# Kernel optimization log

Hardware: AMD Instinct MI355X
Metric: run time of the kernel (lower is better)

Reference implementation:

```python
import jax, jax.numpy as jnp
import numpy as np

B, T, IO = 64, 1024, 1
H = 512
DELAY = 1


def _lstm_cell(x_t, h, c, Wih, Whh, bih, bhh):
    # PyTorch LSTMCell: gates = x@Wih.T + bih + h@Whh.T + bhh, gate order i,f,g,o
    gates = x_t @ Wih.T + bih + h @ Whh.T + bhh  # [B, 4H]
    i, f, g, o = jnp.split(gates, 4, axis=-1)
    i = jax.nn.sigmoid(i)
    f = jax.nn.sigmoid(f)
    g = jnp.tanh(g)
    o = jax.nn.sigmoid(o)
    c_new = f * c + i * g
    h_new = o * jnp.tanh(c_new)
    return h_new, c_new


def setup_inputs() -> dict:
    key = jax.random.key(0)
    ks = jax.random.split(key, 14)
    s = 0.02
    inp = {
        "x": jax.random.normal(ks[0], (B, T, IO), dtype=jnp.float32),
        # layer 0: input IO -> H
        "Wih0": jax.random.normal(ks[1], (4 * H, IO), dtype=jnp.float32) * s,
        "Whh0": jax.random.normal(ks[2], (4 * H, H), dtype=jnp.float32) * s,
        "bih0": jax.random.normal(ks[3], (4 * H,), dtype=jnp.float32) * s,
        "bhh0": jax.random.normal(ks[4], (4 * H,), dtype=jnp.float32) * s,
        # layer 1: H -> H
        "Wih1": jax.random.normal(ks[5], (4 * H, H), dtype=jnp.float32) * s,
        "Whh1": jax.random.normal(ks[6], (4 * H, H), dtype=jnp.float32) * s,
        "bih1": jax.random.normal(ks[7], (4 * H,), dtype=jnp.float32) * s,
        "bhh1": jax.random.normal(ks[8], (4 * H,), dtype=jnp.float32) * s,
        # layer 2: H -> H
        "Wih2": jax.random.normal(ks[9], (4 * H, H), dtype=jnp.float32) * s,
        "Whh2": jax.random.normal(ks[10], (4 * H, H), dtype=jnp.float32) * s,
        "bih2": jax.random.normal(ks[11], (4 * H,), dtype=jnp.float32) * s,
        "bhh2": jax.random.normal(ks[12], (4 * H,), dtype=jnp.float32) * s,
        # output head: H -> IO
        "Wout": jax.random.normal(ks[13], (IO, H), dtype=jnp.float32) * s,
        "bout": jnp.zeros((IO,), dtype=jnp.float32),
    }
    return inp


def reference(x, Wih0, Whh0, bih0, bhh0, Wih1, Whh1, bih1, bhh1,
              Wih2, Whh2, bih2, bhh2, Wout, bout):
    # delay: shift input right by DELAY steps, zero-pad front
    pad = jnp.zeros_like(x[:, :DELAY, :])
    x = jnp.concatenate([pad, x[:, :-DELAY, :]], axis=1)

    h0 = jnp.zeros((x.shape[0], H), dtype=x.dtype)
    carry0 = (h0, h0, h0, h0, h0, h0)  # (h0,c0,h1,c1,h2,c2)

    xs = jnp.swapaxes(x, 0, 1)  # [T, B, IO]

    def step(carry, x_t):
        h0, c0, h1, c1, h2, c2 = carry
        h0, c0 = _lstm_cell(x_t, h0, c0, Wih0, Whh0, bih0, bhh0)
        h1, c1 = _lstm_cell(h0, h1, c1, Wih1, Whh1, bih1, bhh1)
        h2, c2 = _lstm_cell(h1, h2, c2, Wih2, Whh2, bih2, bhh2)
        o_t = h2 @ Wout.T + bout  # [B, IO]
        return (h0, c0, h1, c1, h2, c2), o_t

    _, outs = jax.lax.scan(step, carry0, xs)  # [T, B, IO]
    return jnp.swapaxes(outs, 0, 1)  # [B, T, IO]
```

## Files before the change

### kernel.cpp

```cpp
#include <hip/hip_runtime.h>
#include <stdint.h>

#define Hdim 512
#define Bsz 64
#define Tlen 1024
#define RING 8
#define GR (RING * 16 * Hdim)
#define FSTR 16
#define LROW 516

typedef __attribute__((ext_vector_type(8))) short short8;
typedef __attribute__((ext_vector_type(4))) short bf16x4;
typedef __attribute__((ext_vector_type(4))) float f32x4;
typedef unsigned long long u64;
struct u64x2 { u64 lo, hi; };

__device__ __forceinline__ short f2bf(float f) {
  uint32_t u = __float_as_uint(f);
  u += 0x7fffu + ((u >> 16) & 1u);
  return (short)(u >> 16);
}

__device__ __forceinline__ f32x4 mfma16(short8 a, short8 b, f32x4 c) {
  return __builtin_amdgcn_mfma_f32_16x16x32_bf16(a, b, c, 0, 0, 0);
}

__device__ __forceinline__ void vm_wait0() {
  asm volatile("s_waitcnt vmcnt(0)" ::: "memory");
  __builtin_amdgcn_sched_barrier(0);
}

__device__ __forceinline__ void wait_multi(const uint32_t* pp, uint32_t tgt) {
  uint32_t it = 0;
  for (;;) {
    uint32_t v = __hip_atomic_load(pp, __ATOMIC_RELAXED, __HIP_MEMORY_SCOPE_AGENT);
    if (__all((int)(v >= tgt))) break;
    __builtin_amdgcn_s_sleep(1);
    if (++it > (1u << 20)) break;
  }
}

__device__ __forceinline__ short8 frag_read(const short* __restrict__ lds,
                                            int lane, int ks) {
  int base = (lane & 15) * LROW + (lane >> 4) * 8 + ks * 32;
  bf16x4 lo = *(const bf16x4*)(lds + base);
  bf16x4 hi = *(const bf16x4*)(lds + base + 4);
  short8 r;
  r[0] = lo[0]; r[1] = lo[1]; r[2] = lo[2]; r[3] = lo[3];
  r[4] = hi[0]; r[5] = hi[1]; r[6] = hi[2]; r[7] = hi[3];
  return r;
}

__global__ void out_init(float* out, const float* bout) {
  int i = blockIdx.x * 256 + threadIdx.x;
  if (i < Bsz * Tlen) out[i] = bout[0];
}

__global__ void pack_kernel(const float* __restrict__ Whh0,
                            const float* __restrict__ Wih1, const float* __restrict__ Whh1,
                            const float* __restrict__ Wih2, const float* __restrict__ Whh2,
                            short* __restrict__ Bpack) {
  int ch = blockIdx.x * 256 + threadIdx.x;
  const int L0C = 64 * 16 * 2 * 64;
  const int L12C = 64 * 32 * 2 * 64;
  if (ch >= L0C + 2 * L12C) return;
  int layer, rel, KS;
  const float* Wih;
  const float* Whh;
  if (ch < L0C) { layer = 0; rel = ch; KS = 16; Wih = nullptr; Whh = Whh0; }
  else if (ch < L0C + L12C) { layer = 1; rel = ch - L0C; KS = 32; Wih = Wih1; Whh = Whh1; }
  else { layer = 2; rel = ch - L0C - L12C; KS = 32; Wih = Wih2; Whh = Whh2; }
  int lane = rel & 63;
  int nt = (rel >> 6) & 1;
  int rest = rel >> 7;
  int ks = rest % KS;
  int dw = rest / KS;
  int w = dw & 3;
  int d = dw >> 2;
  int col = nt * 16 + (lane & 15);
  int row = (col >> 3) * Hdim + d * 32 + w * 8 + (col & 7);
  int kbase = ks * 32 + (lane >> 4) * 8;
  short8 v;
#pragma unroll
  for (int e = 0; e < 8; ++e) {
    int k = kbase + e;
    float wt;
    if (layer == 0) wt = Whh[row * Hdim + k];
    else wt = (k < Hdim) ? Wih[row * Hdim + k] : Whh[row * Hdim + (k - Hdim)];
    v[e] = f2bf(wt);
  }
  ((short8*)Bpack)[ch] = v;
}

__global__ __launch_bounds__(256, 1)
void lstm_persist(const float* __restrict__ x,
                  const float* __restrict__ Wih0v,
                  const float* __restrict__ bih0, const float* __restrict__ bhh0,
                  const float* __restrict__ bih1, const float* __restrict__ bhh1,
                  const float* __restrict__ bih2, const float* __restrict__ bhh2,
                  const float* __restrict__ Wout,
                  const short* __restrict__ Bpack,
                  short* __restrict__ rings,
                  uint32_t* __restrict__ flags,
                  float* __restrict__ out) {
  const int blk = blockIdx.x;
  const int layer = blk >> 6;
  const int g = (blk >> 4) & 3;
  const int d = blk & 15;
  const int tid = threadIdx.x;
  const int lane = tid & 63;
  const int wave = tid >> 6;

  __shared__ short ldsA[16 * LROW];
  __shared__ short ldsB[16 * LROW];
  __shared__ short hbuf[16][32];
  __shared__ float pbuf[4][16];

  short8 bw[32][2];
  {
    const short8* bp = (const short8*)Bpack;
    if (layer == 0) {
#pragma unroll
      for (int ks = 0; ks < 16; ++ks) {
        bw[ks][0] = bp[((((d * 4 + wave) * 16 + ks) * 2 + 0) * 64) + lane];
        bw[ks][1] = bp[((((d * 4 + wave) * 16 + ks) * 2 + 1) * 64) + lane];
        asm volatile("" : "+v"(bw[ks][0]), "+v"(bw[ks][1]));
      }
    } else {
      const int base = (layer == 1) ? 131072 : 393216;
#pragma unroll
      for (int ks = 0; ks < 32; ++ks) {
        bw[ks][0] = bp[base + (((d * 4 + wave) * 32 + ks) * 2 + 0) * 64 + lane];
        bw[ks][1] = bp[base + (((d * 4 + wave) * 32 + ks) * 2 + 1) * 64 + lane];
        asm volatile("" : "+v"(bw[ks][0]), "+v"(bw[ks][1]));
      }
    }
  }

  const float* bih = (layer == 0) ? bih0 : (layer == 1 ? bih1 : bih2);
  const float* bhh = (layer == 0) ? bhh0 : (layer == 1 ? bhh1 : bhh2);
  const int dimb = d * 32 + wave * 8 + (lane & 7);
  const int row0 = (((lane & 15) >> 3)) * Hdim + dimb;
  const int row1 = (((lane & 15) >> 3) + 2) * Hdim + dimb;
  const float bias0 = bih[row0] + bhh[row0];
  const float bias1 = bih[row1] + bhh[row1];
  float xw0 = 0.f, xw1 = 0.f, woutd = 0.f;
  if (layer == 0) { xw0 = Wih0v[row0]; xw1 = Wih0v[row1]; }
  if (layer == 2) woutd = Wout[dimb];

  uint32_t* flagsO = flags + ((layer * 4 + g) * 16) * FSTR;
  const uint32_t* flagsP = flags + (((layer - 1) * 4 + g) * 16) * FSTR;
  const uint32_t* flagsN = flags + (((layer + 1) * 4 + g) * 16) * FSTR;
  short* ringLG = rings + (layer * 4 + g) * GR;
  const short* ringPG = rings + ((layer - 1) * 4 + g) * GR;

  const uint32_t* pptr;
  int pmode;
  if (lane < 16) { pptr = flagsO + lane * FSTR; pmode = 0; }
  else if (lane < 32 && layer > 0) { pptr = flagsP + (lane - 16) * FSTR; pmode = 1; }
  else if (lane >= 32 && lane < 48 && layer < 2) { pptr = flagsN + (lane - 32) * FSTR; pmode = 2; }
  else { pptr = flagsO; pmode = 3; }

  const int bR = 4 * (lane >> 4);

  float c[4] = {0.f, 0.f, 0.f, 0.f};

  for (int t = 0; t < Tlen; ++t) {
    if (wave == 0) {
      uint32_t tgt;
      if (pmode == 0) tgt = (uint32_t)t;
      else if (pmode == 1) tgt = (uint32_t)(t + 1);
      else if (pmode == 2) tgt = (t + 1 >= RING) ? (uint32_t)(t + 1 - RING) : 0u;
      else tgt = 0u;
      wait_multi(pptr, tgt);
    }
    __syncthreads();

    {
      const bool doA = (layer > 0);
      const bool doB = (t > 0);
      u64 va[8], vb[8];
      if (doA) {
        const short* srcA = ringPG + (t & (RING - 1)) * (16 * Hdim);
#pragma unroll
        for (int j = 0; j < 4; ++j) {
          const u64* s = (const u64*)(srcA + (wave * 4 + j) * 512);
          va[2 * j]     = __hip_atomic_load(s + lane,      __ATOMIC_RELAXED, __HIP_MEMORY_SCOPE_AGENT);
          va[2 * j + 1] = __hip_atomic_load(s + lane + 64, __ATOMIC_RELAXED, __HIP_MEMORY_SCOPE_AGENT);
        }
      }
      if (doB) {
        const short* srcB = ringLG + ((t - 1) & (RING - 1)) * (16 * Hdim);
#pragma unroll
        for (int j = 0; j < 4; ++j) {
          const u64* s = (const u64*)(srcB + (wave * 4 + j) * 512);
          vb[2 * j]     = __hip_atomic_load(s + lane,      __ATOMIC_RELAXED, __HIP_MEMORY_SCOPE_AGENT);
          vb[2 * j + 1] = __hip_atomic_load(s + lane + 64, __ATOMIC_RELAXED, __HIP_MEMORY_SCOPE_AGENT);
        }
      }
      if (doA) {
#pragma unroll
        for (int j = 0; j < 4; ++j) {
          u64* dst = (u64*)(ldsA + (wave * 4 + j) * LROW);
          dst[lane]      = va[2 * j];
          dst[lane + 64] = va[2 * j + 1];
        }
      }
      if (doB) {
#pragma unroll
        for (int j = 0; j < 4; ++j) {
          u64* dst = (u64*)(ldsB + (wave * 4 + j) * LROW);
          dst[lane]      = vb[2 * j];
          dst[lane + 64] = vb[2 * j + 1];
        }
      }
    }
    __syncthreads();

    f32x4 acc0 = {bias0, bias0, bias0, bias0};
    f32x4 acc1 = {bias1, bias1, bias1, bias1};
    if (layer > 0) {
#pragma unroll
      for (int ks = 0; ks < 16; ++ks) {
        short8 a = frag_read(ldsA, lane, ks);
        acc0 = mfma16(a, bw[ks][0], acc0);
        acc1 = mfma16(a, bw[ks][1], acc1);
      }
    } else if (t > 0) {
#pragma unroll
      for (int r = 0; r < 4; ++r) {
        float xv = x[(g * 16 + bR + r) * Tlen + (t - 1)];
        acc0[r] += xw0 * xv;
        acc1[r] += xw1 * xv;
      }
    }
    if (t > 0) {
      if (layer == 0) {
#pragma unroll
        for (int ks = 0; ks < 16; ++ks) {
          short8 a = frag_read(ldsB, lane, ks);
          acc0 = mfma16(a, bw[ks][0], acc0);
          acc1 = mfma16(a, bw[ks][1], acc1);
        }
      } else {
#pragma unroll
        for (int ks = 0; ks < 16; ++ks) {
          short8 a = frag_read(ldsB, lane, ks);
          acc0 = mfma16(a, bw[16 + ks][0], acc0);
          acc1 = mfma16(a, bw[16 + ks][1], acc1);
        }
      }
    }

    float parts[4];
#pragma unroll
    for (int r = 0; r < 4; ++r) {
      float a0 = acc0[r], a1 = acc1[r];
      float p0 = __shfl_xor(a0, 8);
      float p1 = __shfl_xor(a1, 8);
      float iv = 1.f / (1.f + __expf(-a0));
      float fv = 1.f / (1.f + __expf(-p0));
      float gv = tanhf(a1);
      float ov = 1.f / (1.f + __expf(-p1));
      c[r] = fv * c[r] + iv * gv;
      float hv = ov * tanhf(c[r]);
      if ((lane & 8) == 0) hbuf[bR + r][wave * 8 + (lane & 7)] = f2bf(hv);
      parts[r] = hv * woutd;
    }
    if (layer == 2) {
#pragma unroll
      for (int r = 0; r < 4; ++r) {
        parts[r] += __shfl_xor(parts[r], 1);
        parts[r] += __shfl_xor(parts[r], 2);
        parts[r] += __shfl_xor(parts[r], 4);
        if ((lane & 15) == 0) pbuf[wave][bR + r] = parts[r];
      }
    }

    __syncthreads();
    {
      short* hout = ringLG + (t & (RING - 1)) * (16 * Hdim);
      if (tid < 128) {
        int row = tid >> 3, cch = tid & 7;
        u64 v = ((const u64*)&hbuf[row][0])[cch];
        u64* dst = (u64*)(hout + row * Hdim + d * 32) + cch;
        __hip_atomic_store(dst, v, __ATOMIC_RELAXED, __HIP_MEMORY_SCOPE_AGENT);
      }
      vm_wait0();
      __syncthreads();
      if (tid == 0)
        __hip_atomic_store(flagsO + d * FSTR, (uint32_t)(t + 1), __ATOMIC_RELAXED,
                           __HIP_MEMORY_SCOPE_AGENT);
      if (layer == 2 && wave == 0 && lane < 16) {
        float s = pbuf[0][lane] + pbuf[1][lane] + pbuf[2][lane] + pbuf[3][lane];
        atomicAdd(out + (g * 16 + lane) * Tlen + t, s);
      }
    }
  }
}

extern "C" void kernel_launch(void* const* d_in, const int* in_sizes, int n_in,
                              void* d_out, int out_size, void* d_ws, size_t ws_size,
                              hipStream_t stream) {
  const float* x    = (const float*)d_in[0];
  const float* Wih0 = (const float*)d_in[1];
  const float* Whh0 = (const float*)d_in[2];
  const float* bih0 = (const float*)d_in[3];
  const float* bhh0 = (const float*)d_in[4];
  const float* Wih1 = (const float*)d_in[5];
  const float* Whh1 = (const float*)d_in[6];
  const float* bih1 = (const float*)d_in[7];
  const float* bhh1 = (const float*)d_in[8];
  const float* Wih2 = (const float*)d_in[9];
  const float* Whh2 = (const float*)d_in[10];
  const float* bih2 = (const float*)d_in[11];
  const float* bhh2 = (const float*)d_in[12];
  const float* Wout = (const float*)d_in[13];
  const float* bout = (const float*)d_in[14];

  char* ws = (char*)d_ws;
  short* Bpack    = (short*)ws;
  short* rings    = (short*)(ws + 10485760);
  uint32_t* flags = (uint32_t*)(ws + 12058624);
  float* out      = (float*)d_out;

  (void)hipMemsetAsync(flags, 0, 12 * 16 * FSTR * sizeof(uint32_t), stream);
  out_init<<<(Bsz * Tlen + 255) / 256, 256, 0, stream>>>(out, bout);
  pack_kernel<<<2560, 256, 0, stream>>>(Whh0, Wih1, Whh1, Wih2, Whh2, Bpack);
  lstm_persist<<<192, 256, 0, stream>>>(x, Wih0, bih0, bhh0, bih1, bhh1, bih2, bhh2,
                                        Wout, Bpack, rings, flags, out);
}
```

Measured before the change: 5.163 ms.

## Tighten per-step cross-block handoff with wide cache-bypassing loads and single-wave publish

Replaces the per-lane 64-bit atomic ring loads with eight 128-bit global loads issued in inline assembly with sc0 sc1 cache-coherence bits, then writes them to LDS as 128-bit stores. The LDS row pad grows so fragment reads become a single 128-bit access. The hidden-state publish is done by one wave with 128-bit stores followed by an immediate flag store, which removes one block-wide barrier. The spin-wait drops its sleep, the flag polling moves to wave 1, and the output atomic moves to wave 2 so these jobs spread across waves. It also always loads both halves, including useless loads for layer 0 and t=0, and relies on the sc0 sc1 bits plus vmcnt waits for visibility of data across blocks.

Result: no change. 5.191 ms (median of 3 runs) (+0.6%).

```diff
diff --git a/kernel.cpp b/kernel.cpp
--- a/kernel.cpp
+++ b/kernel.cpp
@@ -7,13 +7,12 @@
 #define RING 8
 #define GR (RING * 16 * Hdim)
 #define FSTR 16
-#define LROW 516
+#define LROW 520
 
 typedef __attribute__((ext_vector_type(8))) short short8;
-typedef __attribute__((ext_vector_type(4))) short bf16x4;
+typedef __attribute__((ext_vector_type(4))) int i32x4;
 typedef __attribute__((ext_vector_type(4))) float f32x4;
 typedef unsigned long long u64;
-struct u64x2 { u64 lo, hi; };
 
 __device__ __forceinline__ short f2bf(float f) {
   uint32_t u = __float_as_uint(f);
@@ -23,11 +22,6 @@
 
 __device__ __forceinline__ f32x4 mfma16(short8 a, short8 b, f32x4 c) {
   return __builtin_amdgcn_mfma_f32_16x16x32_bf16(a, b, c, 0, 0, 0);
-}
-
-__device__ __forceinline__ void vm_wait0() {
-  asm volatile("s_waitcnt vmcnt(0)" ::: "memory");
-  __builtin_amdgcn_sched_barrier(0);
 }
 
 __device__ __forceinline__ void wait_multi(const uint32_t* pp, uint32_t tgt) {
@@ -35,20 +29,53 @@
   for (;;) {
     uint32_t v = __hip_atomic_load(pp, __ATOMIC_RELAXED, __HIP_MEMORY_SCOPE_AGENT);
     if (__all((int)(v >= tgt))) break;
-    __builtin_amdgcn_s_sleep(1);
-    if (++it > (1u << 20)) break;
+    if (++it > (1u << 22)) break;
   }
+}
+
+__device__ __forceinline__ void stage_both(const short* __restrict__ srcA,
+                                           const short* __restrict__ srcB,
+                                           short* __restrict__ ldsA,
+                                           short* __restrict__ ldsB,
+                                           int wave, int lane) {
+  const int r0 = wave * 4;
+  const short* pa0 = srcA + (r0 + 0) * 512 + lane * 8;
+  const short* pa1 = srcA + (r0 + 1) * 512 + lane * 8;
+  const short* pa2 = srcA + (r0 + 2) * 512 + lane * 8;
+  const short* pa3 = srcA + (r0 + 3) * 512 + lane * 8;
+  const short* pb0 = srcB + (r0 + 0) * 512 + lane * 8;
+  const short* pb1 = srcB + (r0 + 1) * 512 + lane * 8;
+  const short* pb2 = srcB + (r0 + 2) * 512 + lane * 8;
+  const short* pb3 = srcB + (r0 + 3) * 512 + lane * 8;
+  i32x4 t0, t1, t2, t3, t4, t5, t6, t7;
+  asm volatile(
+      "global_load_dwordx4 %0, %8, off sc0 sc1\n\t"
+      "global_load_dwordx4 %1, %9, off sc0 sc1\n\t"
+      "global_load_dwordx4 %2, %10, off sc0 sc1\n\t"
+      "global_load_dwordx4 %3, %11, off sc0 sc1\n\t"
+      "global_load_dwordx4 %4, %12, off sc0 sc1\n\t"
+      "global_load_dwordx4 %5, %13, off sc0 sc1\n\t"
+      "global_load_dwordx4 %6, %14, off sc0 sc1\n\t"
+      "global_load_dwordx4 %7, %15, off sc0 sc1\n\t"
+      "s_waitcnt vmcnt(0)"
+      : "=&v"(t0), "=&v"(t1), "=&v"(t2), "=&v"(t3),
+        "=&v"(t4), "=&v"(t5), "=&v"(t6), "=&v"(t7)
+      : "v"(pa0), "v"(pa1), "v"(pa2), "v"(pa3),
+        "v"(pb0), "v"(pb1), "v"(pb2), "v"(pb3)
+      : "memory");
+  *(i32x4*)(ldsA + (r0 + 0) * LROW + lane * 8) = t0;
+  *(i32x4*)(ldsA + (r0 + 1) * LROW + lane * 8) = t1;
+  *(i32x4*)(ldsA + (r0 + 2) * LROW + lane * 8) = t2;
+  *(i32x4*)(ldsA + (r0 + 3) * LROW + lane * 8) = t3;
+  *(i32x4*)(ldsB + (r0 + 0) * LROW + lane * 8) = t4;
+  *(i32x4*)(ldsB + (r0 + 1) * LROW + lane * 8) = t5;
+  *(i32x4*)(ldsB + (r0 + 2) * LROW + lane * 8) = t6;
+  *(i32x4*)(ldsB + (r0 + 3) * LROW + lane * 8) = t7;
 }
 
 __device__ __forceinline__ short8 frag_read(const short* __restrict__ lds,
                                             int lane, int ks) {
-  int base = (lane & 15) * LROW + (lane >> 4) * 8 + ks * 32;
-  bf16x4 lo = *(const bf16x4*)(lds + base);
-  bf16x4 hi = *(const bf16x4*)(lds + base + 4);
-  short8 r;
-  r[0] = lo[0]; r[1] = lo[1]; r[2] = lo[2]; r[3] = lo[3];
-  r[4] = hi[0]; r[5] = hi[1]; r[6] = hi[2]; r[7] = hi[3];
-  return r;
+  return *(const short8*)(lds + (lane & 15) * LROW + (lane >> 4) * 8 + ks * 32);
 }
 
 __global__ void out_init(float* out, const float* bout) {
@@ -166,7 +193,7 @@
   float c[4] = {0.f, 0.f, 0.f, 0.f};
 
   for (int t = 0; t < Tlen; ++t) {
-    if (wave == 0) {
+    if (wave == 1) {
       uint32_t tgt;
       if (pmode == 0) tgt = (uint32_t)t;
       else if (pmode == 1) tgt = (uint32_t)(t + 1);
@@ -177,43 +204,9 @@
     __syncthreads();
 
     {
-      const bool doA = (layer > 0);
-      const bool doB = (t > 0);
-      u64 va[8], vb[8];
-      if (doA) {
-        const short* srcA = ringPG + (t & (RING - 1)) * (16 * Hdim);
-#pragma unroll
-        for (int j = 0; j < 4; ++j) {
-          const u64* s = (const u64*)(srcA + (wave * 4 + j) * 512);
-          va[2 * j]     = __hip_atomic_load(s + lane,      __ATOMIC_RELAXED, __HIP_MEMORY_SCOPE_AGENT);
-          va[2 * j + 1] = __hip_atomic_load(s + lane + 64, __ATOMIC_RELAXED, __HIP_MEMORY_SCOPE_AGENT);
-        }
-      }
-      if (doB) {
-        const short* srcB = ringLG + ((t - 1) & (RING - 1)) * (16 * Hdim);
-#pragma unroll
-        for (int j = 0; j < 4; ++j) {
-          const u64* s = (const u64*)(srcB + (wave * 4 + j) * 512);
-          vb[2 * j]     = __hip_atomic_load(s + lane,      __ATOMIC_RELAXED, __HIP_MEMORY_SCOPE_AGENT);
-          vb[2 * j + 1] = __hip_atomic_load(s + lane + 64, __ATOMIC_RELAXED, __HIP_MEMORY_SCOPE_AGENT);
-        }
-      }
-      if (doA) {
-#pragma unroll
-        for (int j = 0; j < 4; ++j) {
-          u64* dst = (u64*)(ldsA + (wave * 4 + j) * LROW);
-          dst[lane]      = va[2 * j];
-          dst[lane + 64] = va[2 * j + 1];
-        }
-      }
-      if (doB) {
-#pragma unroll
-        for (int j = 0; j < 4; ++j) {
-          u64* dst = (u64*)(ldsB + (wave * 4 + j) * LROW);
-          dst[lane]      = vb[2 * j];
-          dst[lane + 64] = vb[2 * j + 1];
-        }
-      }
+      const short* srcA = (layer > 0) ? ringPG + (t & (RING - 1)) * (16 * Hdim) : ringLG;
+      const short* srcB = (t > 0) ? ringLG + ((t - 1) & (RING - 1)) * (16 * Hdim) : srcA;
+      stage_both(srcA, srcB, ldsA, ldsB, wave, lane);
     }
     __syncthreads();
 
@@ -278,23 +271,22 @@
     }
 
     __syncthreads();
-    {
+
+    if (wave == 0) {
       short* hout = ringLG + (t & (RING - 1)) * (16 * Hdim);
-      if (tid < 128) {
-        int row = tid >> 3, cch = tid & 7;
-        u64 v = ((const u64*)&hbuf[row][0])[cch];
-        u64* dst = (u64*)(hout + row * Hdim + d * 32) + cch;
-        __hip_atomic_store(dst, v, __ATOMIC_RELAXED, __HIP_MEMORY_SCOPE_AGENT);
-      }
-      vm_wait0();
-      __syncthreads();
-      if (tid == 0)
+      int row = lane >> 2, q = lane & 3;
+      i32x4 v = *(const i32x4*)&hbuf[row][q * 8];
+      short* dst = hout + row * Hdim + d * 32 + q * 8;
+      asm volatile("global_store_dwordx4 %0, %1, off sc0 sc1\n\t"
+                   "s_waitcnt vmcnt(0)"
+                   :: "v"(dst), "v"(v) : "memory");
+      if (lane == 0)
         __hip_atomic_store(flagsO + d * FSTR, (uint32_t)(t + 1), __ATOMIC_RELAXED,
                            __HIP_MEMORY_SCOPE_AGENT);
-      if (layer == 2 && wave == 0 && lane < 16) {
-        float s = pbuf[0][lane] + pbuf[1][lane] + pbuf[2][lane] + pbuf[3][lane];
-        atomicAdd(out + (g * 16 + lane) * Tlen + t, s);
-      }
+    }
+    if (layer == 2 && wave == 2 && lane < 16) {
+      float s = pbuf[0][lane] + pbuf[1][lane] + pbuf[2][lane] + pbuf[3][lane];
+      atomicAdd(out + (g * 16 + lane) * Tlen + t, s);
     }
   }
 }
```
